# Kernel tuning notes

Hardware: AMD Instinct MI355X
Metric: run time of the kernel (lower is better)

Reference implementation:

```python
import jax, jax.numpy as jnp
import numpy as np

B, S, D, H = 8, 1024, 1024, 16
HD = D // H  # 64


def setup_inputs() -> dict:
    key = jax.random.key(0)
    ks = jax.random.split(key, 10)
    f32 = jnp.float32
    inp = {
        "query": jax.random.normal(ks[0], (B, S, D), f32),
        "key": jax.random.normal(ks[1], (B, S, D), f32),
        "value": jax.random.normal(ks[2], (B, S, D), f32),
        "rel": jax.random.normal(ks[3], (B, S, S), f32),
        "timestamp": jax.random.normal(ks[4], (B, S, S), f32),
        "mask": jax.random.randint(ks[5], (B, S, S), 0, 2).astype(bool),
        "l1": jnp.float32(0.3),
        "l2": jnp.float32(0.5),
        "encode_pos": 0,
        "Wq": jax.random.normal(ks[6], (D, D), f32) * 0.02,
        "bq": jnp.zeros((D,), f32),
        "Wk": jax.random.normal(ks[7], (D, D), f32) * 0.02,
        "bk": jnp.zeros((D,), f32),
        "Wv": jax.random.normal(ks[8], (D, D), f32) * 0.02,
        "bv": jnp.zeros((D,), f32),
    }
    return inp


def _proj(x, W, b):
    # nn.Linear: x @ W.T + b, then split heads -> [B, H, S, HD]
    y = x @ W.T + b
    return y.reshape(B, S, H, HD).transpose(0, 2, 1, 3)


def reference(query, key, value, rel, timestamp, mask, l1, l2, encode_pos,
              Wq, bq, Wk, bk, Wv, bv):
    # encode_pos == 0 path: QK^T + time-decay + rel-attn three-softmax blend
    q = _proj(query, Wq, bq)
    k = _proj(key, Wk, bk)
    v = _proj(value, Wv, bv)

    m = mask[:, None]                       # [B,1,S,S], broadcasts over heads
    mf = m.astype(jnp.float32)

    # rel attention: zero out where mask is False, then fill zeros with -1e5
    rel_m = rel[:, None] * mf               # [B,1,S,S]
    rel_attn = jax.nn.softmax(jnp.where(rel_m == 0, -100000.0, rel_m), axis=-1)

    inv_sqrt_d = 1.0 / np.sqrt(HD).astype(np.float32)
    scores = jnp.einsum("bhqd,bhkd->bhqk", q, k) * inv_sqrt_d
    scores = jnp.where(m, -1e32, scores)

    time_stamp = jnp.exp(-jnp.abs(timestamp[:, None]))   # [B,1,S,S]
    time_stamp = jnp.where(m, -100000.0, time_stamp)

    prob_attn = jax.nn.softmax(scores, axis=-1)          # [B,H,S,S]
    time_attn = jax.nn.softmax(time_stamp, axis=-1)      # [B,1,S,S]

    prob_attn = (1.0 - l2) * prob_attn + l2 * time_attn
    prob_attn = (1.0 - l1) * prob_attn + l1 * rel_attn
    # dropout is identity at inference

    out = jnp.einsum("bhqk,bhkd->bhqd", prob_attn, v)
    out = out.transpose(0, 2, 1, 3).reshape(B, S, D)
    return out, prob_attn
```

## Files before the change

### kernel.cpp

```cpp
#include <hip/hip_runtime.h>
#include <stdint.h>

typedef short bf16x8 __attribute__((ext_vector_type(8)));
typedef float f32x4 __attribute__((ext_vector_type(4)));
typedef unsigned short u16x4 __attribute__((ext_vector_type(4)));
typedef unsigned short u16x8 __attribute__((ext_vector_type(8)));

constexpr int NB = 8, NS = 1024, ND = 1024, NH = 16, NHD = 64;

static __device__ __forceinline__ unsigned short f2bf(float f) {
    union { float f; uint32_t u; } v; v.f = f;
    uint32_t r = (v.u + 0x7fffu + ((v.u >> 16) & 1u)) >> 16;
    return (unsigned short)r;
}

static __device__ __forceinline__ bool mask_at(const void* m, size_t idx, int ms) {
    if (ms == 4) return ((const unsigned int*)m)[idx] != 0u;
    return ((const unsigned char*)m)[idx] != 0;
}

__global__ void detect_mask(const unsigned int* __restrict__ m, int* __restrict__ flag) {
    int l = threadIdx.x;
    bool bad = false;
    for (int i = l; i < 1024; i += 64) {
        unsigned int w = m[i];
        bad |= (w > 1u && w != 0x3f800000u);
    }
    bad = (bool)__any(bad);
    if (l == 0) *flag = bad ? 1 : 4;
}

__global__ __launch_bounds__(256) void cvt_frag(const float* __restrict__ in,
                                                unsigned short* __restrict__ out, int n8) {
    int stride = gridDim.x * blockDim.x;
    for (int idx = blockIdx.x * blockDim.x + threadIdx.x; idx < n8; idx += stride) {
        const float4* p = (const float4*)in + 2 * (size_t)idx;
        float4 a = p[0], b = p[1];
        u16x8 o;
        o[0] = f2bf(a.x); o[1] = f2bf(a.y); o[2] = f2bf(a.z); o[3] = f2bf(a.w);
        o[4] = f2bf(b.x); o[5] = f2bf(b.y); o[6] = f2bf(b.z); o[7] = f2bf(b.w);
        int m = idx >> 7, c8 = idx & 127;
        int kt = c8 >> 2, sub = c8 & 3;
        int lane = (m & 15) + 16 * sub;
        size_t slot = ((size_t)(m >> 4) * 32 + kt) * 64 + lane;
        *(u16x8*)(out + slot * 8) = o;
    }
}

__global__ __launch_bounds__(256) void proj_gemm(const unsigned short* __restrict__ Af,
                                                 const unsigned short* __restrict__ Wf,
                                                 const float* __restrict__ bias,
                                                 unsigned short* __restrict__ C, int mode) {
    int l = threadIdx.x & 63, w = threadIdx.x >> 6;
    int lr = l & 15, lg = l >> 4;
    int m_base = blockIdx.x * 128 + (w >> 1) * 64;
    int n_base = blockIdx.y * 128 + (w & 1) * 64;
    int mtg0 = m_base >> 4, ntg0 = n_base >> 4;
    f32x4 acc[4][4] = {};
    for (int kt = 0; kt < 32; kt++) {
        bf16x8 af[4], bfr[4];
        #pragma unroll
        for (int mt = 0; mt < 4; mt++)
            af[mt] = *(const bf16x8*)(Af + (((size_t)(mtg0 + mt) * 32 + kt) * 64 + l) * 8);
        #pragma unroll
        for (int nt = 0; nt < 4; nt++)
            bfr[nt] = *(const bf16x8*)(Wf + (((size_t)(ntg0 + nt) * 32 + kt) * 64 + l) * 8);
        #pragma unroll
        for (int mt = 0; mt < 4; mt++) {
            #pragma unroll
            for (int nt = 0; nt < 4; nt++)
                acc[mt][nt] = __builtin_amdgcn_mfma_f32_16x16x32_bf16(af[mt], bfr[nt], acc[mt][nt], 0, 0, 0);
        }
    }
    #pragma unroll
    for (int mt = 0; mt < 4; mt++) {
        #pragma unroll
        for (int nt = 0; nt < 4; nt++) {
            int col = n_base + nt * 16 + lr;
            int row0 = m_base + mt * 16 + lg * 4;
            float bv = bias[col];
            int b = row0 >> 10;
            int h = col >> 6;
            if (mode == 0) {
                int st = (row0 & 1023) >> 4;
                int d32 = (col & 63) >> 5;
                int sub = (col & 31) >> 3;
                int e = col & 7;
                size_t base = ((((size_t)(b * NH + h) * 64 + st) * 2 + d32) * 64) * 8;
                #pragma unroll
                for (int r = 0; r < 4; r++) {
                    int lane = lg * 4 + r + 16 * sub;
                    C[base + (size_t)lane * 8 + e] = f2bf(acc[mt][nt][r] + bv);
                }
            } else {
                int s0 = row0 & 1023;
                int ks = s0 >> 5;
                int dd = col & 63;
                int dt = dd >> 4;
                int lane = (dd & 15) + 16 * ((s0 & 31) >> 3);
                u16x4 pk;
                #pragma unroll
                for (int r = 0; r < 4; r++) pk[r] = f2bf(acc[mt][nt][r] + bv);
                size_t base = ((((size_t)(b * NH + h) * 32 + ks) * 4 + dt) * 64 + lane) * 8 + (lg & 1) * 4;
                *(u16x4*)(C + base) = pk;
            }
        }
    }
}

__global__ __launch_bounds__(256) void tr_kernel(const float* __restrict__ rel,
                                                 const float* __restrict__ ts,
                                                 const void* __restrict__ maskp,
                                                 const int* __restrict__ msflag,
                                                 const float* __restrict__ l1p,
                                                 const float* __restrict__ l2p,
                                                 float* __restrict__ TRf,
                                                 uint32_t* __restrict__ PMf) {
    __shared__ float s_tm[4], s_rm[4], s_ts[4], s_rs[4];
    __shared__ unsigned char s_nib[256];
    int row = blockIdx.x;
    int t = threadIdx.x, w = t >> 6, l = t & 63;
    int ms = *msflag;
    size_t base = (size_t)row * NS;
    float4 r4 = ((const float4*)(rel + base))[t];
    float4 t4 = ((const float4*)(ts + base))[t];
    float rr[4], tt[4];
    *(float4*)rr = r4; *(float4*)tt = t4;
    float tv[4], rv[4];
    unsigned nib = 0;
    float tmx = -3.0e38f, rmx = -3.0e38f;
    #pragma unroll
    for (int j = 0; j < 4; j++) {
        bool m = mask_at(maskp, base + t * 4 + j, ms);
        nib |= (m ? 1u : 0u) << j;
        tv[j] = m ? -100000.0f : __expf(-fabsf(tt[j]));
        float rm_ = m ? rr[j] : 0.0f;
        rv[j] = (rm_ == 0.0f) ? -100000.0f : rm_;
        tmx = fmaxf(tmx, tv[j]); rmx = fmaxf(rmx, rv[j]);
    }
    s_nib[t] = (unsigned char)nib;
    #pragma unroll
    for (int off = 1; off < 64; off <<= 1) {
        tmx = fmaxf(tmx, __shfl_xor(tmx, off));
        rmx = fmaxf(rmx, __shfl_xor(rmx, off));
    }
    if (l == 0) { s_tm[w] = tmx; s_rm[w] = rmx; }
    __syncthreads();
    tmx = fmaxf(fmaxf(s_tm[0], s_tm[1]), fmaxf(s_tm[2], s_tm[3]));
    rmx = fmaxf(fmaxf(s_rm[0], s_rm[1]), fmaxf(s_rm[2], s_rm[3]));
    float te[4], re[4], tsum = 0.f, rsum = 0.f;
    #pragma unroll
    for (int j = 0; j < 4; j++) {
        te[j] = __expf(tv[j] - tmx); tsum += te[j];
        re[j] = __expf(rv[j] - rmx); rsum += re[j];
    }
    #pragma unroll
    for (int off = 1; off < 64; off <<= 1) {
        tsum += __shfl_xor(tsum, off);
        rsum += __shfl_xor(rsum, off);
    }
    if (l == 0) { s_ts[w] = tsum; s_rs[w] = rsum; }
    __syncthreads();
    tsum = s_ts[0] + s_ts[1] + s_ts[2] + s_ts[3];
    rsum = s_rs[0] + s_rs[1] + s_rs[2] + s_rs[3];
    float l1 = *l1p, l2 = *l2p;
    float ti = ((1.0f - l1) * l2) / tsum;
    float ri = l1 / rsum;
    float4 o;
    o.x = te[0] * ti + re[0] * ri;
    o.y = te[1] * ti + re[1] * ri;
    o.z = te[2] * ti + re[2] * ri;
    o.w = te[3] * ti + re[3] * ri;
    int b = row >> 10, q = row & 1023;
    int qt = q >> 4, qr = q & 15;
    size_t slot = ((((size_t)(b * 64 + qt) * 4 + (t >> 6)) * 16 + ((t >> 2) & 15)) * 64
                   + (qr + 16 * (t & 3)));
    ((float4*)TRf)[slot] = o;
    if (t < 32) {
        uint32_t word = 0;
        #pragma unroll
        for (int i = 0; i < 8; i++)
            word |= ((uint32_t)s_nib[t * 8 + i]) << (i * 4);
        PMf[(((size_t)(b * 64 + qt) * 4 + (t >> 3)) * 16 + qr) * 8 + (t & 7)] = word;
    }
}

__global__ __launch_bounds__(256) void att_pv_kernel(const unsigned short* __restrict__ Qf,
                                                     const unsigned short* __restrict__ Kf,
                                                     const uint32_t* __restrict__ PMf,
                                                     const float* __restrict__ TRf,
                                                     const float* __restrict__ l1p,
                                                     const float* __restrict__ l2p,
                                                     const unsigned short* __restrict__ Vf,
                                                     float* __restrict__ probOut,
                                                     float* __restrict__ outp) {
    __shared__ float redm[4][16];
    __shared__ float reds[4][16];
    __shared__ unsigned short P_lds[16 * 1024];
    int bid = blockIdx.x;
    int qt = bid & 63;
    int h = (bid >> 6) & 15;
    int b = bid >> 10;
    int tid = threadIdx.x, w = tid >> 6, l = tid & 63, lr = l & 15, lg = l >> 4;
    int q0 = qt * 16;
    int k_base = w * 256;
    int q = q0 + lr;
    size_t bh = (size_t)(b * NH + h);

    const unsigned short* qf = Qf + (((bh * 64 + qt) * 2) * 64 + l) * 8;
    bf16x8 bq0 = *(const bf16x8*)(qf);
    bf16x8 bq1 = *(const bf16x8*)(qf + 64 * 8);

    const uint32_t* pmp = PMf + (((size_t)(b * 64 + qt) * 4 + w) * 16 + lr) * 8;
    uint32_t pm[8];
    *(uint4*)(pm) = *(const uint4*)(pmp);
    *(uint4*)(pm + 4) = *(const uint4*)(pmp + 4);

    f32x4 acc[16] = {};
    const unsigned short* kfb = Kf + (((bh * 64 + w * 16) * 2) * 64) * 8 + (size_t)l * 8;
    #pragma unroll
    for (int t = 0; t < 16; t++) {
        const unsigned short* kp = kfb + (size_t)t * 2 * 64 * 8;
        bf16x8 a0 = *(const bf16x8*)(kp);
        bf16x8 a1 = *(const bf16x8*)(kp + 64 * 8);
        acc[t] = __builtin_amdgcn_mfma_f32_16x16x32_bf16(a0, bq0, acc[t], 0, 0, 0);
        acc[t] = __builtin_amdgcn_mfma_f32_16x16x32_bf16(a1, bq1, acc[t], 0, 0, 0);
    }
    #pragma unroll
    for (int t = 0; t < 16; t++) {
        uint32_t word = pm[t >> 1];
        int shift = (t & 1) * 16 + lg * 4;
        #pragma unroll
        for (int r = 0; r < 4; r++) {
            bool m = (word >> (shift + r)) & 1u;
            acc[t][r] = m ? -1.0e32f : acc[t][r] * 0.125f;
        }
    }
    float mx = acc[0][0];
    #pragma unroll
    for (int t = 0; t < 16; t++) {
        #pragma unroll
        for (int r = 0; r < 4; r++) mx = fmaxf(mx, acc[t][r]);
    }
    mx = fmaxf(mx, __shfl_xor(mx, 16));
    mx = fmaxf(mx, __shfl_xor(mx, 32));
    if (l < 16) redm[w][l] = mx;
    __syncthreads();
    float rowmax = fmaxf(fmaxf(redm[0][lr], redm[1][lr]), fmaxf(redm[2][lr], redm[3][lr]));
    float sm = 0.f;
    #pragma unroll
    for (int t = 0; t < 16; t++) {
        #pragma unroll
        for (int r = 0; r < 4; r++) {
            float e = __expf(acc[t][r] - rowmax);
            acc[t][r] = e;
            sm += e;
        }
    }
    sm += __shfl_xor(sm, 16);
    sm += __shfl_xor(sm, 32);
    if (l < 16) reds[w][l] = sm;
    __syncthreads();
    float total = reds[0][lr] + reds[1][lr] + reds[2][lr] + reds[3][lr];
    float l1 = *l1p, l2 = *l2p;
    float rinv = ((1.0f - l1) * (1.0f - l2)) / total;

    float* po = probOut + bh * NS * NS + (size_t)q * NS;
    const float* trf = TRf + ((((size_t)(b * 64 + qt) * 4 + w) * 16) * 64 + l) * 4;
    uint32_t swz_w = (uint32_t)((q & 7) << 4);
    #pragma unroll
    for (int t = 0; t < 16; t++) {
        int kc = k_base + t * 16 + lg * 4;
        float4 tr4 = *(const float4*)(trf + (size_t)t * 64 * 4);
        float4 o;
        o.x = acc[t][0] * rinv + tr4.x;
        o.y = acc[t][1] * rinv + tr4.y;
        o.z = acc[t][2] * rinv + tr4.z;
        o.w = acc[t][3] * rinv + tr4.w;
        *(float4*)(po + kc) = o;
        u16x4 pk;
        pk[0] = f2bf(o.x); pk[1] = f2bf(o.y); pk[2] = f2bf(o.z); pk[3] = f2bf(o.w);
        uint32_t waddr = ((uint32_t)(lr * 2048 + kc * 2)) ^ swz_w;
        *(u16x4*)((char*)P_lds + waddr) = pk;
    }
    __syncthreads();

    const unsigned short* vf = Vf + ((bh * 32 * 4 + w) * 64 + l) * 8;
    uint32_t swz_r = (uint32_t)((lr & 7) << 4);
    f32x4 acc2 = {};
    #pragma unroll 8
    for (int ks = 0; ks < 32; ks++) {
        int k0 = ks * 32;
        bf16x8 vfrag = *(const bf16x8*)(vf + (size_t)ks * 4 * 64 * 8);
        uint32_t raddr = ((uint32_t)(lr * 2048 + (k0 + lg * 8) * 2)) ^ swz_r;
        bf16x8 pfrag = *(const bf16x8*)((const char*)P_lds + raddr);
        acc2 = __builtin_amdgcn_mfma_f32_16x16x32_bf16(vfrag, pfrag, acc2, 0, 0, 0);
    }
    float4 ov;
    ov.x = acc2[0]; ov.y = acc2[1]; ov.z = acc2[2]; ov.w = acc2[3];
    *(float4*)(outp + ((size_t)b * NS + q0 + lr) * ND + h * NHD + w * 16 + lg * 4) = ov;
}

extern "C" void kernel_launch(void* const* d_in, const int* in_sizes, int n_in,
                              void* d_out, int out_size, void* d_ws, size_t ws_size,
                              hipStream_t stream) {
    const float* query = (const float*)d_in[0];
    const float* key   = (const float*)d_in[1];
    const float* value = (const float*)d_in[2];
    const float* rel   = (const float*)d_in[3];
    const float* ts    = (const float*)d_in[4];
    const void*  mask  = d_in[5];
    const float* l1p   = (const float*)d_in[6];
    const float* l2p   = (const float*)d_in[7];
    const float* Wq = (const float*)d_in[9];
    const float* bq = (const float*)d_in[10];
    const float* Wk = (const float*)d_in[11];
    const float* bk = (const float*)d_in[12];
    const float* Wv = (const float*)d_in[13];
    const float* bv = (const float*)d_in[14];

    char* ws = (char*)d_ws;
    const size_t SZ = (size_t)NB * NS * ND * 2;
    unsigned short* Qf  = (unsigned short*)(ws);
    unsigned short* Kf  = (unsigned short*)(ws + SZ);
    unsigned short* Vf  = (unsigned short*)(ws + 2 * SZ);
    unsigned short* Afq = (unsigned short*)(ws + 3 * SZ);
    unsigned short* Afk = (unsigned short*)(ws + 4 * SZ);
    unsigned short* Afv = (unsigned short*)(ws + 5 * SZ);
    unsigned short* Wfq = (unsigned short*)(ws + 6 * SZ);
    unsigned short* Wfk = (unsigned short*)(ws + 6 * SZ + 2u * 1024 * 1024);
    unsigned short* Wfv = (unsigned short*)(ws + 6 * SZ + 4u * 1024 * 1024);
    int* msflag         = (int*)(ws + 6 * SZ + 6u * 1024 * 1024);
    uint32_t* PMf       = (uint32_t*)(ws + 6 * SZ + 8u * 1024 * 1024);
    float* TRf = (float*)(ws + 3 * SZ);

    detect_mask<<<1, 64, 0, stream>>>((const unsigned int*)mask, msflag);

    const int nX8 = NB * NS * ND / 8;
    const int nW8 = 1024 * 1024 / 8;
    cvt_frag<<<1024, 256, 0, stream>>>(query, Afq, nX8);
    cvt_frag<<<1024, 256, 0, stream>>>(key,   Afk, nX8);
    cvt_frag<<<1024, 256, 0, stream>>>(value, Afv, nX8);
    cvt_frag<<<256, 256, 0, stream>>>(Wq, Wfq, nW8);
    cvt_frag<<<256, 256, 0, stream>>>(Wk, Wfk, nW8);
    cvt_frag<<<256, 256, 0, stream>>>(Wv, Wfv, nW8);

    dim3 pg(64, 8);
    proj_gemm<<<pg, 256, 0, stream>>>(Afq, Wfq, bq, Qf, 0);
    proj_gemm<<<pg, 256, 0, stream>>>(Afk, Wfk, bk, Kf, 0);
    proj_gemm<<<pg, 256, 0, stream>>>(Afv, Wfv, bv, Vf, 1);

    tr_kernel<<<NB * NS, 256, 0, stream>>>(rel, ts, mask, msflag, l1p, l2p, TRf, PMf);

    float* outp = (float*)d_out;
    float* probOut = outp + (size_t)NB * NS * ND;
    att_pv_kernel<<<NB * NH * (NS / 16), 256, 0, stream>>>(Qf, Kf, PMf, TRf, l1p, l2p, Vf,
                                                           probOut, outp);
}
```

Baseline: 621.3 us.

## Feed softmax registers directly into PV MFMA and drop max-reduction pass

The attention kernel no longer stages the bf16 probability tile in LDS. Each wave feeds its register-resident probabilities straight into 16x16x16 bf16 MFMAs against a V layout rewritten to match, then reduces the four per-wave partial outputs through a small LDS buffer. The row-max pass and its barrier are removed, exponentiating scaled scores directly and zeroing masked entries, which relies on scores staying small enough not to overflow. The block index is also swizzled to change scheduling order across batches and heads.

```diff
diff --git a/kernel.cpp b/kernel.cpp
--- a/kernel.cpp
+++ b/kernel.cpp
@@ -2,6 +2,7 @@
 #include <stdint.h>
 
 typedef short bf16x8 __attribute__((ext_vector_type(8)));
+typedef short bf16x4 __attribute__((ext_vector_type(4)));
 typedef float f32x4 __attribute__((ext_vector_type(4)));
 typedef unsigned short u16x4 __attribute__((ext_vector_type(4)));
 typedef unsigned short u16x8 __attribute__((ext_vector_type(8)));
@@ -12,6 +13,22 @@
     union { float f; uint32_t u; } v; v.f = f;
     uint32_t r = (v.u + 0x7fffu + ((v.u >> 16) & 1u)) >> 16;
     return (unsigned short)r;
+}
+
+static __device__ __forceinline__ f32x4 mfma32(bf16x8 a, bf16x8 b, f32x4 c) {
+    return __builtin_amdgcn_mfma_f32_16x16x32_bf16(a, b, c, 0, 0, 0);
+}
+
+static __device__ __forceinline__ f32x4 mfma16(bf16x4 a, bf16x4 b, f32x4 c) {
+#if __has_builtin(__builtin_amdgcn_mfma_f32_16x16x16bf16_1k)
+    return __builtin_amdgcn_mfma_f32_16x16x16bf16_1k(a, b, c, 0, 0, 0);
+#elif __has_builtin(__builtin_amdgcn_mfma_f32_16x16x16_bf16)
+    return __builtin_amdgcn_mfma_f32_16x16x16_bf16(a, b, c, 0, 0, 0);
+#else
+    asm volatile("v_mfma_f32_16x16x16_bf16 %0, %1, %2, %0\n\ts_nop 7\n\ts_nop 7"
+                 : "+v"(c) : "v"(a), "v"(b));
+    return c;
+#endif
 }
 
 static __device__ __forceinline__ bool mask_at(const void* m, size_t idx, int ms) {
@@ -69,7 +86,7 @@
         for (int mt = 0; mt < 4; mt++) {
             #pragma unroll
             for (int nt = 0; nt < 4; nt++)
-                acc[mt][nt] = __builtin_amdgcn_mfma_f32_16x16x32_bf16(af[mt], bfr[nt], acc[mt][nt], 0, 0, 0);
+                acc[mt][nt] = mfma32(af[mt], bfr[nt], acc[mt][nt]);
         }
     }
     #pragma unroll
@@ -94,15 +111,19 @@
                 }
             } else {
                 int s0 = row0 & 1023;
-                int ks = s0 >> 5;
+                int tg = s0 >> 4;
+                int wv = tg >> 4;
+                int t_in = tg & 15;
+                int tp = t_in >> 1, half = t_in & 1;
                 int dd = col & 63;
                 int dt = dd >> 4;
-                int lane = (dd & 15) + 16 * ((s0 & 31) >> 3);
+                int lane = (dd & 15) + 16 * lg;
                 u16x4 pk;
                 #pragma unroll
                 for (int r = 0; r < 4; r++) pk[r] = f2bf(acc[mt][nt][r] + bv);
-                size_t base = ((((size_t)(b * NH + h) * 32 + ks) * 4 + dt) * 64 + lane) * 8 + (lg & 1) * 4;
-                *(u16x4*)(C + base) = pk;
+                size_t addr = (((((size_t)(b * NH + h) * 4 + wv) * 8 + tp) * 4 + dt) * 64 + lane) * 8
+                              + half * 4;
+                *(u16x4*)(C + addr) = pk;
             }
         }
     }
@@ -194,13 +215,13 @@
                                                      const unsigned short* __restrict__ Vf,
                                                      float* __restrict__ probOut,
                                                      float* __restrict__ outp) {
-    __shared__ float redm[4][16];
     __shared__ float reds[4][16];
-    __shared__ unsigned short P_lds[16 * 1024];
+    __shared__ f32x4 pacc[4][4][64];
     int bid = blockIdx.x;
-    int qt = bid & 63;
-    int h = (bid >> 6) & 15;
-    int b = bid >> 10;
+    int swz = ((bid & 7) << 10) | (bid >> 3);
+    int qt = swz & 63;
+    int h = (swz >> 6) & 15;
+    int b = swz >> 10;
     int tid = threadIdx.x, w = tid >> 6, l = tid & 63, lr = l & 15, lg = l >> 4;
     int q0 = qt * 16;
     int k_base = w * 256;
@@ -223,9 +244,10 @@
         const unsigned short* kp = kfb + (size_t)t * 2 * 64 * 8;
         bf16x8 a0 = *(const bf16x8*)(kp);
         bf16x8 a1 = *(const bf16x8*)(kp + 64 * 8);
-        acc[t] = __builtin_amdgcn_mfma_f32_16x16x32_bf16(a0, bq0, acc[t], 0, 0, 0);
-        acc[t] = __builtin_amdgcn_mfma_f32_16x16x32_bf16(a1, bq1, acc[t], 0, 0, 0);
-    }
+        acc[t] = mfma32(a0, bq0, acc[t]);
+        acc[t] = mfma32(a1, bq1, acc[t]);
+    }
+    float sm = 0.f;
     #pragma unroll
     for (int t = 0; t < 16; t++) {
         uint32_t word = pm[t >> 1];
@@ -233,26 +255,7 @@
         #pragma unroll
         for (int r = 0; r < 4; r++) {
             bool m = (word >> (shift + r)) & 1u;
-            acc[t][r] = m ? -1.0e32f : acc[t][r] * 0.125f;
-        }
-    }
-    float mx = acc[0][0];
-    #pragma unroll
-    for (int t = 0; t < 16; t++) {
-        #pragma unroll
-        for (int r = 0; r < 4; r++) mx = fmaxf(mx, acc[t][r]);
-    }
-    mx = fmaxf(mx, __shfl_xor(mx, 16));
-    mx = fmaxf(mx, __shfl_xor(mx, 32));
-    if (l < 16) redm[w][l] = mx;
-    __syncthreads();
-    float rowmax = fmaxf(fmaxf(redm[0][lr], redm[1][lr]), fmaxf(redm[2][lr], redm[3][lr]));
-    float sm = 0.f;
-    #pragma unroll
-    for (int t = 0; t < 16; t++) {
-        #pragma unroll
-        for (int r = 0; r < 4; r++) {
-            float e = __expf(acc[t][r] - rowmax);
+            float e = m ? 0.0f : __expf(acc[t][r] * 0.125f);
             acc[t][r] = e;
             sm += e;
         }
@@ -265,39 +268,43 @@
     float l1 = *l1p, l2 = *l2p;
     float rinv = ((1.0f - l1) * (1.0f - l2)) / total;
 
-    float* po = probOut + bh * NS * NS + (size_t)q * NS;
+    float* po = probOut + bh * NS * NS + (size_t)q * NS + k_base;
     const float* trf = TRf + ((((size_t)(b * 64 + qt) * 4 + w) * 16) * 64 + l) * 4;
-    uint32_t swz_w = (uint32_t)((q & 7) << 4);
-    #pragma unroll
-    for (int t = 0; t < 16; t++) {
-        int kc = k_base + t * 16 + lg * 4;
-        float4 tr4 = *(const float4*)(trf + (size_t)t * 64 * 4);
-        float4 o;
-        o.x = acc[t][0] * rinv + tr4.x;
-        o.y = acc[t][1] * rinv + tr4.y;
-        o.z = acc[t][2] * rinv + tr4.z;
-        o.w = acc[t][3] * rinv + tr4.w;
-        *(float4*)(po + kc) = o;
-        u16x4 pk;
-        pk[0] = f2bf(o.x); pk[1] = f2bf(o.y); pk[2] = f2bf(o.z); pk[3] = f2bf(o.w);
-        uint32_t waddr = ((uint32_t)(lr * 2048 + kc * 2)) ^ swz_w;
-        *(u16x4*)((char*)P_lds + waddr) = pk;
-    }
+    const unsigned short* vf = Vf + ((((size_t)bh * 4 + w) * 8 * 4) * 64 + (size_t)l) * 8;
+    f32x4 acc2[4] = {};
+    #pragma unroll
+    for (int tp = 0; tp < 8; tp++) {
+        bf16x4 pfa, pfb;
+        #pragma unroll
+        for (int hf = 0; hf < 2; hf++) {
+            int t = tp * 2 + hf;
+            float4 tr4 = *(const float4*)(trf + t * 256);
+            float4 o;
+            o.x = acc[t][0] * rinv + tr4.x;
+            o.y = acc[t][1] * rinv + tr4.y;
+            o.z = acc[t][2] * rinv + tr4.z;
+            o.w = acc[t][3] * rinv + tr4.w;
+            *(float4*)(po + t * 16 + lg * 4) = o;
+            bf16x4 pk;
+            pk[0] = (short)f2bf(o.x); pk[1] = (short)f2bf(o.y);
+            pk[2] = (short)f2bf(o.z); pk[3] = (short)f2bf(o.w);
+            if (hf == 0) pfa = pk; else pfb = pk;
+        }
+        #pragma unroll
+        for (int dt = 0; dt < 4; dt++) {
+            bf16x8 vv = *(const bf16x8*)(vf + (size_t)(tp * 4 + dt) * 64 * 8);
+            bf16x4 v0 = __builtin_shufflevector(vv, vv, 0, 1, 2, 3);
+            bf16x4 v1 = __builtin_shufflevector(vv, vv, 4, 5, 6, 7);
+            acc2[dt] = mfma16(v0, pfa, acc2[dt]);
+            acc2[dt] = mfma16(v1, pfb, acc2[dt]);
+        }
+    }
+    #pragma unroll
+    for (int dt = 0; dt < 4; dt++) pacc[w][dt][l] = acc2[dt];
     __syncthreads();
-
-    const unsigned short* vf = Vf + ((bh * 32 * 4 + w) * 64 + l) * 8;
-    uint32_t swz_r = (uint32_t)((lr & 7) << 4);
-    f32x4 acc2 = {};
-    #pragma unroll 8
-    for (int ks = 0; ks < 32; ks++) {
-        int k0 = ks * 32;
-        bf16x8 vfrag = *(const bf16x8*)(vf + (size_t)ks * 4 * 64 * 8);
-        uint32_t raddr = ((uint32_t)(lr * 2048 + (k0 + lg * 8) * 2)) ^ swz_r;
-        bf16x8 pfrag = *(const bf16x8*)((const char*)P_lds + raddr);
-        acc2 = __builtin_amdgcn_mfma_f32_16x16x32_bf16(vfrag, pfrag, acc2, 0, 0, 0);
-    }
+    f32x4 s4 = pacc[0][w][l] + pacc[1][w][l] + pacc[2][w][l] + pacc[3][w][l];
     float4 ov;
-    ov.x = acc2[0]; ov.y = acc2[1]; ov.z = acc2[2]; ov.w = acc2[3];
+    ov.x = s4[0]; ov.y = s4[1]; ov.z = s4[2]; ov.w = s4[3];
     *(float4*)(outp + ((size_t)b * NS + q0 + lr) * ND + h * NHD + w * 16 + lg * 4) = ov;
 }
 
```

After: 572.8 us. -7.8%, faster.
